# Kernel tuning notes

Measured on AMD Instinct MI355X. Metric: run time of the kernel, lower is better.

Reference implementation:

```python
import jax, jax.numpy as jnp
import numpy as np
import math

EMBED = 1024
HEADS = 16
HEAD_DIM = EMBED // HEADS
B, S = 4, 2048
FF = 4 * EMBED
EPS = 1e-5


def _layernorm(x, g, b):
    mu = jnp.mean(x, axis=-1, keepdims=True)
    var = jnp.mean(jnp.square(x - mu), axis=-1, keepdims=True)
    return (x - mu) * jax.lax.rsqrt(var + EPS) * g + b


def setup_inputs() -> dict:
    key = jax.random.key(0)
    ks = jax.random.split(key, 12)
    sd_e = 1.0 / math.sqrt(EMBED)
    sd_ff = 1.0 / math.sqrt(FF)
    return {
        "x": jax.random.normal(ks[0], (B, S, EMBED), jnp.float32),
        # attention weights stored [in, out] (transposed torch Linear)
        "Wq": jax.random.normal(ks[1], (EMBED, EMBED), jnp.float32) * sd_e,
        "bq": jnp.zeros((EMBED,), jnp.float32),
        "Wk": jax.random.normal(ks[2], (EMBED, EMBED), jnp.float32) * sd_e,
        "bk": jnp.zeros((EMBED,), jnp.float32),
        "Wv": jax.random.normal(ks[3], (EMBED, EMBED), jnp.float32) * sd_e,
        "bv": jnp.zeros((EMBED,), jnp.float32),
        "Wo": jax.random.normal(ks[4], (EMBED, EMBED), jnp.float32) * sd_e,
        "bo": jnp.zeros((EMBED,), jnp.float32),
        "g1": jnp.ones((EMBED,), jnp.float32),
        "beta1": jnp.zeros((EMBED,), jnp.float32),
        "g2": jnp.ones((EMBED,), jnp.float32),
        "beta2": jnp.zeros((EMBED,), jnp.float32),
        "W1": jax.random.normal(ks[5], (EMBED, FF), jnp.float32) * sd_e,
        "b1": jnp.zeros((FF,), jnp.float32),
        "W2": jax.random.normal(ks[6], (FF, EMBED), jnp.float32) * sd_ff,
        "b2": jnp.zeros((EMBED,), jnp.float32),
    }


def reference(x, Wq, bq, Wk, bk, Wv, bv, Wo, bo, g1, beta1, g2, beta2, W1, b1, W2, b2):
    b, s, _ = x.shape
    # --- pre-LN causal self-attention (dropout in eval = identity) ---
    h = _layernorm(x, g1, beta1)
    q = (h @ Wq + bq).reshape(b, s, HEADS, HEAD_DIM)
    k = (h @ Wk + bk).reshape(b, s, HEADS, HEAD_DIM)
    v = (h @ Wv + bv).reshape(b, s, HEADS, HEAD_DIM)
    scores = jnp.einsum("bqhd,bkhd->bhqk", q, k) / math.sqrt(HEAD_DIM)
    causal = jnp.tril(jnp.ones((s, s), bool))
    scores = jnp.where(causal, scores, jnp.float32(-1e8))
    attn = jax.nn.softmax(scores, axis=-1)
    y = jnp.einsum("bhqk,bkhd->bqhd", attn, v).reshape(b, s, EMBED)
    x = x + (y @ Wo + bo)
    # --- GELU MLP (exact erf gelu, torch default) ---
    h2 = _layernorm(x, g2, beta2)
    ff = jax.nn.gelu(h2 @ W1 + b1, approximate=False) @ W2 + b2
    return x + ff
```

## Files before the change

### kernel.cpp

```cpp
#include <hip/hip_runtime.h>
#include <hip/hip_bf16.h>
#include <stdint.h>
#include <math.h>

#define SEQ 2048
#define NTOK 8192
#define EMB 1024
#define NH 16
#define HD 64
#define FFD 4096

using us = unsigned short;
using b8 = __attribute__((ext_vector_type(8))) __bf16;
using f4 = __attribute__((ext_vector_type(4))) float;

__device__ __forceinline__ us f2b(float f) {
  union { float f; uint32_t u; } v; v.f = f;
  uint32_t u = v.u;
  return (us)((u + 0x7fffu + ((u >> 16) & 1u)) >> 16);
}

__device__ __forceinline__ uint32_t pkbf(float a, float b) {
  union { float f; uint32_t u; } x, y; x.f = a; y.f = b;
  return ((x.u + 0x8000u) >> 16) | ((y.u + 0x8000u) & 0xFFFF0000u);
}

__device__ __forceinline__ void async16(void* lds, const void* g) {
  __builtin_amdgcn_global_load_lds(
      (__attribute__((address_space(1))) void*)(uintptr_t)g,
      (__attribute__((address_space(3))) void*)(uintptr_t)lds, 16, 0, 0);
}

#define FENCED_BARRIER() do { asm volatile("" ::: "memory"); \
  __builtin_amdgcn_s_barrier(); asm volatile("" ::: "memory"); } while (0)

__device__ __forceinline__ float gelu_f(float x) {
  const float z = -2.30211416f * x * (1.f + 0.044715f * x * x);
  return x / (1.f + __builtin_amdgcn_exp2f(z));
}

__global__ __launch_bounds__(256)
void transpose_cast(const float* __restrict__ in, us* __restrict__ out, int R, int C) {
  __shared__ float tile[32][33];
  const int bc = blockIdx.x * 32, br = blockIdx.y * 32;
  const int tx = threadIdx.x & 31, ty = threadIdx.x >> 5;
#pragma unroll
  for (int i = 0; i < 32; i += 8)
    tile[ty + i][tx] = in[(size_t)(br + ty + i) * C + bc + tx];
  __syncthreads();
#pragma unroll
  for (int i = 0; i < 32; i += 8)
    out[(size_t)(bc + ty + i) * R + br + tx] = f2b(tile[tx][ty + i]);
}

__global__ void pack_bias(const float* __restrict__ bq, const float* __restrict__ bk,
                          const float* __restrict__ bv, float* __restrict__ o) {
  int i = blockIdx.x * 256 + threadIdx.x;
  o[i] = (i < 1024) ? bq[i] : (i < 2048 ? bk[i - 1024] : bv[i - 2048]);
}

__global__ __launch_bounds__(256)
void ln_kernel(const float* __restrict__ x, const float* __restrict__ g,
               const float* __restrict__ be, us* __restrict__ out) {
  __shared__ float red[8];
  const int row = blockIdx.x, t = threadIdx.x;
  const float4 v = ((const float4*)(x + (size_t)row * EMB))[t];
  float s = v.x + v.y + v.z + v.w;
  float s2 = v.x * v.x + v.y * v.y + v.z * v.z + v.w * v.w;
#pragma unroll
  for (int o = 32; o; o >>= 1) { s += __shfl_down(s, o, 64); s2 += __shfl_down(s2, o, 64); }
  if ((t & 63) == 0) { red[(t >> 6) * 2] = s; red[(t >> 6) * 2 + 1] = s2; }
  __syncthreads();
  const float ts = red[0] + red[2] + red[4] + red[6];
  const float ts2 = red[1] + red[3] + red[5] + red[7];
  const float mu = ts * (1.f / 1024.f);
  const float rs = rsqrtf(ts2 * (1.f / 1024.f) - mu * mu + 1e-5f);
  const float4 gv = ((const float4*)g)[t];
  const float4 bv = ((const float4*)be)[t];
  ushort4 o4;
  o4.x = f2b((v.x - mu) * rs * gv.x + bv.x);
  o4.y = f2b((v.y - mu) * rs * gv.y + bv.y);
  o4.z = f2b((v.z - mu) * rs * gv.z + bv.z);
  o4.w = f2b((v.w - mu) * rs * gv.w + bv.w);
  ((ushort4*)(out + (size_t)row * EMB))[t] = o4;
}

template<int BN>
__global__ __launch_bounds__(512, 2)
void gemm8(const us* __restrict__ A, const us* __restrict__ Bt,
           const float* __restrict__ bias, const float* __restrict__ resid,
           float* __restrict__ outF, us* __restrict__ outB,
           int M, int N, int K, int gelu, int gy) {
  constexpr int NF = BN / 64;
  constexpr int BROWS = BN / 8;
  constexpr int BINSTS = BN / 64;
  __shared__ us As[2][256 * 64];
  __shared__ us Bs[2][BN * 64];

  int bid = blockIdx.x;
  const int cpx = (int)gridDim.x >> 3;
  bid = (bid & 7) * cpx + (bid >> 3);
  const int bx = bid / gy, by = bid - bx * gy;
  const int row0 = bx * 256, col0 = by * BN;

  const int tid = threadIdx.x, w = tid >> 6, lane = tid & 63;
  const int wm = w >> 2, wn = w & 3;
  const int quad = lane >> 4, l15 = lane & 15;

  const int srow = lane >> 3;
  const int soct = (lane & 7) ^ srow;
  const us* Ag = A + (size_t)(row0 + w * 32 + srow) * K + soct * 8;
  const us* Bg = Bt + (size_t)(col0 + w * BROWS + srow) * K + soct * 8;
  const int NT = K >> 6;

  const f4 zf = {0.f, 0.f, 0.f, 0.f};
  f4 acc[8][NF];
#pragma unroll
  for (int i = 0; i < 8; i++)
#pragma unroll
    for (int j = 0; j < NF; j++) acc[i][j] = zf;

  auto STAGE = [&](int buf, int t) {
    const size_t ko = (size_t)t * 64;
#pragma unroll
    for (int i = 0; i < 4; i++)
      async16(&As[buf][(w * 32 + i * 8) * 64], Ag + ko + (size_t)(i * 8) * K);
#pragma unroll
    for (int i = 0; i < BINSTS; i++)
      async16(&Bs[buf][(w * BROWS + i * 8) * 64], Bg + ko + (size_t)(i * 8) * K);
  };

  STAGE(0, 0);
  STAGE(1, 1);
  if constexpr (BN == 256) asm volatile("s_waitcnt vmcnt(8)" ::: "memory");
  else                     asm volatile("s_waitcnt vmcnt(6)" ::: "memory");
  FENCED_BARRIER();

  const int xr = l15 & 7;
  for (int u = 0; u < NT; u++) {
    const int cb = u & 1;
    const us* __restrict__ as = As[cb];
    const us* __restrict__ bs = Bs[cb];
    b8 bf[2][NF];
#pragma unroll
    for (int s = 0; s < 2; s++)
#pragma unroll
      for (int nf = 0; nf < NF; nf++)
        bf[s][nf] = *(const b8*)&bs[(wn * (NF * 16) + nf * 16 + l15) * 64 +
                                    ((((s << 2) + quad) ^ xr) << 3)];
#pragma unroll
    for (int qm = 0; qm < 2; qm++) {
      b8 af[2][4];
#pragma unroll
      for (int s = 0; s < 2; s++)
#pragma unroll
        for (int mi = 0; mi < 4; mi++)
          af[s][mi] = *(const b8*)&as[(wm * 128 + qm * 64 + mi * 16 + l15) * 64 +
                                      ((((s << 2) + quad) ^ xr) << 3)];
      __builtin_amdgcn_s_setprio(1);
#pragma unroll
      for (int s = 0; s < 2; s++)
#pragma unroll
        for (int mi = 0; mi < 4; mi++)
#pragma unroll
          for (int nf = 0; nf < NF; nf++)
            acc[qm * 4 + mi][nf] = __builtin_amdgcn_mfma_f32_16x16x32_bf16(
                af[s][mi], bf[s][nf], acc[qm * 4 + mi][nf], 0, 0, 0);
      __builtin_amdgcn_s_setprio(0);
    }
    asm volatile("s_waitcnt lgkmcnt(0)" ::: "memory");
    FENCED_BARRIER();
    if (u + 2 < NT) {
      STAGE(cb, u + 2);
      if constexpr (BN == 256) asm volatile("s_waitcnt vmcnt(8)" ::: "memory");
      else                     asm volatile("s_waitcnt vmcnt(6)" ::: "memory");
    } else {
      asm volatile("s_waitcnt vmcnt(0)" ::: "memory");
    }
    if (u + 1 < NT) FENCED_BARRIER();
  }

#pragma unroll
  for (int mi8 = 0; mi8 < 8; mi8++) {
#pragma unroll
    for (int nf = 0; nf < NF; nf++) {
      const int gcol = col0 + wn * (NF * 16) + nf * 16 + l15;
      const float bc = bias[gcol];
#pragma unroll
      for (int r = 0; r < 4; r++) {
        const int grow = row0 + wm * 128 + mi8 * 16 + quad * 4 + r;
        float v = acc[mi8][nf][r] + bc;
        if (resid) v += resid[(size_t)grow * N + gcol];
        if (gelu) v = gelu_f(v);
        if (outF) outF[(size_t)grow * N + gcol] = v;
        if (outB) outB[(size_t)grow * N + gcol] = f2b(v);
      }
    }
  }
}

__global__ __launch_bounds__(256, 3)
void attn(const us* __restrict__ qkv, us* __restrict__ y) {
  static const signed char QTM[16] = {15,14,13,12, 10,11,8,9, 5,4,7,6, 0,1,2,3};
  const int bx = blockIdx.x;
  const int bh = bx & 63;
  const int qt = QTM[(bx >> 6) & 15];
  const int bb = bh >> 4, h = bh & 15;
  const int tid = threadIdx.x;
  const int wave = tid >> 6, lane = tid & 63;
  const int quad = lane >> 4, l15 = lane & 15;

  __shared__ us Ks[128 * 64];
  __shared__ us Vt[64 * 132];

  const size_t base = (size_t)bb * SEQ * 3072;
  const int q0 = qt * 128;

  b8 bqf[2][2];
#pragma unroll
  for (int qg = 0; qg < 2; qg++) {
    const us* qp = qkv + base + (size_t)(q0 + wave * 32 + qg * 16 + l15) * 3072 + h * 64 + quad * 8;
    bqf[qg][0] = *(const b8*)qp;
    bqf[qg][1] = *(const b8*)(qp + 32);
  }

  const f4 zf = {0.f, 0.f, 0.f, 0.f};
  f4 o[2][4];
  float mrow[2], lrow[2];
#pragma unroll
  for (int qg = 0; qg < 2; qg++) {
    mrow[qg] = -3.0e38f; lrow[qg] = 0.f;
#pragma unroll
    for (int dg = 0; dg < 4; dg++) o[qg][dg] = zf;
  }

  const int klr = lane >> 3, klc = lane & 7;
  const us* kgbase = qkv + base + (size_t)(wave * 32 + klr) * 3072 + 1024 + h * 64 + ((klc ^ klr) << 3);
  const us* vgbase = qkv + base + (size_t)(2 * lane) * 3072 + 2048 + h * 64 + wave * 8;

  const float sm_scale = 0.125f * 1.44269504088896340736f;

  for (int kt = 0; kt <= qt; kt++) {
    const size_t koff = (size_t)kt * 128 * 3072;
#pragma unroll
    for (int op = 0; op < 4; op++)
      async16(&Ks[(wave * 32 + op * 8) * 64], kgbase + koff + (size_t)op * 8 * 3072);
    {
      union { float4 f; us u[8]; } v0, v1, v2, v3;
      v0.f = *(const float4*)(vgbase + koff);
      v1.f = *(const float4*)(vgbase + koff + 3072);
      v2.f = *(const float4*)(vgbase + koff + 32);
      v3.f = *(const float4*)(vgbase + koff + 3072 + 32);
#pragma unroll
      for (int j = 0; j < 8; j++) {
        *(uint32_t*)&Vt[(wave * 8 + j) * 132 + 2 * lane] =
            (uint32_t)v0.u[j] | ((uint32_t)v1.u[j] << 16);
        *(uint32_t*)&Vt[(32 + wave * 8 + j) * 132 + 2 * lane] =
            (uint32_t)v2.u[j] | ((uint32_t)v3.u[j] << 16);
      }
    }
    __syncthreads();

    f4 sacc[2][8];
#pragma unroll
    for (int c = 0; c < 8; c++) {
      const int krow = (c * 16 + l15) * 64;
      const int sw = l15 & 7;
      const b8 ak0 = *(const b8*)&Ks[krow + ((quad ^ sw) << 3)];
      const b8 ak1 = *(const b8*)&Ks[krow + (((quad ^ 4) ^ sw) << 3)];
#pragma unroll
      for (int qg = 0; qg < 2; qg++) {
        f4 s = __builtin_amdgcn_mfma_f32_16x16x32_bf16(ak0, bqf[qg][0], zf, 0, 0, 0);
        sacc[qg][c] = __builtin_amdgcn_mfma_f32_16x16x32_bf16(ak1, bqf[qg][1], s, 0, 0, 0);
      }
    }

    uint32_t pf[2][16];
    float alpha[2];
#pragma unroll
    for (int qg = 0; qg < 2; qg++) {
      const int q_in = wave * 32 + qg * 16 + l15;
#pragma unroll
      for (int c = 0; c < 8; c++)
#pragma unroll
        for (int r = 0; r < 4; r++) {
          float v = sacc[qg][c][r] * sm_scale;
          if (kt == qt && (c * 16 + quad * 4 + r) > q_in) v = -3.0e38f;
          sacc[qg][c][r] = v;
        }
      float mx = sacc[qg][0][0];
#pragma unroll
      for (int c = 0; c < 8; c++)
#pragma unroll
        for (int r = 0; r < 4; r++) mx = fmaxf(mx, sacc[qg][c][r]);
      mx = fmaxf(mx, __shfl_xor(mx, 16, 64));
      mx = fmaxf(mx, __shfl_xor(mx, 32, 64));
      const float mnew = fmaxf(mrow[qg], mx);
      alpha[qg] = __builtin_amdgcn_exp2f(mrow[qg] - mnew);
      mrow[qg] = mnew;
      float rs = 0.f;
#pragma unroll
      for (int c = 0; c < 8; c++) {
        const float p0 = __builtin_amdgcn_exp2f(sacc[qg][c][0] - mnew);
        const float p1 = __builtin_amdgcn_exp2f(sacc[qg][c][1] - mnew);
        const float p2 = __builtin_amdgcn_exp2f(sacc[qg][c][2] - mnew);
        const float p3 = __builtin_amdgcn_exp2f(sacc[qg][c][3] - mnew);
        rs += (p0 + p1) + (p2 + p3);
        pf[qg][c * 2] = pkbf(p0, p1);
        pf[qg][c * 2 + 1] = pkbf(p2, p3);
      }
      rs += __shfl_xor(rs, 16, 64);
      rs += __shfl_xor(rs, 32, 64);
      lrow[qg] = lrow[qg] * alpha[qg] + rs;
#pragma unroll
      for (int r = 0; r < 4; r++) {
        const float ar = __shfl(alpha[qg], quad * 4 + r, 64);
#pragma unroll
        for (int dg = 0; dg < 4; dg++) o[qg][dg][r] *= ar;
      }
    }

#pragma unroll
    for (int c = 0; c < 8; c++) {
      union { uint32_t w[4]; b8 v; } af0, af1;
      af0.w[0] = pf[0][c * 2]; af0.w[1] = pf[0][c * 2 + 1]; af0.w[2] = 0u; af0.w[3] = 0u;
      af1.w[0] = pf[1][c * 2]; af1.w[1] = pf[1][c * 2 + 1]; af1.w[2] = 0u; af1.w[3] = 0u;
#pragma unroll
      for (int dg = 0; dg < 4; dg++) {
        const uint2 vd = *(const uint2*)&Vt[(dg * 16 + l15) * 132 + c * 16 + quad * 4];
        union { uint32_t w[4]; b8 v; } vb;
        vb.w[0] = vd.x; vb.w[1] = vd.y; vb.w[2] = 0u; vb.w[3] = 0u;
        o[0][dg] = __builtin_amdgcn_mfma_f32_16x16x32_bf16(af0.v, vb.v, o[0][dg], 0, 0, 0);
        o[1][dg] = __builtin_amdgcn_mfma_f32_16x16x32_bf16(af1.v, vb.v, o[1][dg], 0, 0, 0);
      }
    }
    __syncthreads();
  }

#pragma unroll
  for (int qg = 0; qg < 2; qg++) {
    float lr[4];
#pragma unroll
    for (int r = 0; r < 4; r++) lr[r] = __shfl(lrow[qg], quad * 4 + r, 64);
#pragma unroll
    for (int dg = 0; dg < 4; dg++)
#pragma unroll
      for (int r = 0; r < 4; r++) {
        const int gq = q0 + wave * 32 + qg * 16 + quad * 4 + r;
        y[(size_t)(bb * SEQ + gq) * EMB + h * 64 + dg * 16 + l15] = f2b(o[qg][dg][r] / lr[r]);
      }
  }
}

extern "C" void kernel_launch(void* const* d_in, const int* in_sizes, int n_in,
                              void* d_out, int out_size, void* d_ws, size_t ws_size,
                              hipStream_t stream) {
  const float* x = (const float*)d_in[0];
  const float* Wq = (const float*)d_in[1];
  const float* bq = (const float*)d_in[2];
  const float* Wk = (const float*)d_in[3];
  const float* bk = (const float*)d_in[4];
  const float* Wv = (const float*)d_in[5];
  const float* bv = (const float*)d_in[6];
  const float* Wo = (const float*)d_in[7];
  const float* bo = (const float*)d_in[8];
  const float* g1 = (const float*)d_in[9];
  const float* be1 = (const float*)d_in[10];
  const float* g2 = (const float*)d_in[11];
  const float* be2 = (const float*)d_in[12];
  const float* W1 = (const float*)d_in[13];
  const float* b1 = (const float*)d_in[14];
  const float* W2 = (const float*)d_in[15];
  const float* b2 = (const float*)d_in[16];
  float* out = (float*)d_out;

  char* ws = (char*)d_ws;
  const size_t MB = 1024ull * 1024ull;
  us* WqkvT = (us*)(ws + 0);
  us* WoT   = (us*)(ws + 6 * MB);
  us* W1T   = (us*)(ws + 8 * MB);
  us* W2T   = (us*)(ws + 16 * MB);
  us* hbuf  = (us*)(ws + 24 * MB);
  us* qkvb  = (us*)(ws + 40 * MB);
  us* ybuf  = (us*)(ws + 88 * MB);
  float* x1 = (float*)(ws + 104 * MB);
  us* h2    = (us*)(ws + 136 * MB);
  us* ff1   = (us*)(ws + 24 * MB);
  float* bqkv = (float*)(ws + 152 * MB);

  transpose_cast<<<dim3(32, 32), 256, 0, stream>>>(Wq, WqkvT, 1024, 1024);
  transpose_cast<<<dim3(32, 32), 256, 0, stream>>>(Wk, WqkvT + 1024 * 1024, 1024, 1024);
  transpose_cast<<<dim3(32, 32), 256, 0, stream>>>(Wv, WqkvT + 2 * 1024 * 1024, 1024, 1024);
  transpose_cast<<<dim3(32, 32), 256, 0, stream>>>(Wo, WoT, 1024, 1024);
  transpose_cast<<<dim3(128, 32), 256, 0, stream>>>(W1, W1T, 1024, 4096);
  transpose_cast<<<dim3(32, 128), 256, 0, stream>>>(W2, W2T, 4096, 1024);
  pack_bias<<<12, 256, 0, stream>>>(bq, bk, bv, bqkv);

  ln_kernel<<<NTOK, 256, 0, stream>>>(x, g1, be1, hbuf);
  gemm8<128><<<dim3(32 * 24), 512, 0, stream>>>(hbuf, WqkvT, bqkv, nullptr, nullptr, qkvb,
                                                NTOK, 3072, 1024, 0, 24);
  attn<<<1024, 256, 0, stream>>>(qkvb, ybuf);
  gemm8<128><<<dim3(32 * 8), 512, 0, stream>>>(ybuf, WoT, bo, x, x1, nullptr,
                                               NTOK, 1024, 1024, 0, 8);
  ln_kernel<<<NTOK, 256, 0, stream>>>(x1, g2, be2, h2);
  gemm8<256><<<dim3(32 * 16), 512, 0, stream>>>(h2, W1T, b1, nullptr, nullptr, ff1,
                                                NTOK, 4096, 1024, 1, 16);
  gemm8<128><<<dim3(32 * 8), 512, 0, stream>>>(ff1, W2T, b2, x1, out, nullptr,
                                               NTOK, 1024, 4096, 0, 8);
}
```

Measured before the change: 570.8 us.

## Split GEMM into 256x256 and 128x256 kernels with quarter-tile interleaved staging

Replaces the templated gemm8 with two specialized kernels. gemm256 handles the QKV and FFN1 projections with 256x256 tiles (QKV previously used 256x128). gemm128 handles the Wo and FFN2 projections with 128x256 tiles. Each K-step is split into sub-phases that issue async global loads for the next tiles between MFMA groups, with a barrier around each phase, so memory traffic overlaps compute. The epilogues are also specialized. The trade-off is more barriers per K-step, more complex vmcnt accounting, and different grid sizes and wave counts for the smaller-N GEMMs.

```diff
diff --git a/kernel.cpp b/kernel.cpp
--- a/kernel.cpp
+++ b/kernel.cpp
@@ -85,118 +85,294 @@
   ((ushort4*)(out + (size_t)row * EMB))[t] = o4;
 }
 
-template<int BN>
 __global__ __launch_bounds__(512, 2)
-void gemm8(const us* __restrict__ A, const us* __restrict__ Bt,
-           const float* __restrict__ bias, const float* __restrict__ resid,
-           float* __restrict__ outF, us* __restrict__ outB,
-           int M, int N, int K, int gelu, int gy) {
-  constexpr int NF = BN / 64;
-  constexpr int BROWS = BN / 8;
-  constexpr int BINSTS = BN / 64;
+void gemm256(const us* __restrict__ A, const us* __restrict__ Bt,
+             const float* __restrict__ bias, us* __restrict__ outB,
+             int N, int K, int gelu, int gy) {
   __shared__ us As[2][256 * 64];
-  __shared__ us Bs[2][BN * 64];
+  __shared__ us Bs[2][256 * 64];
 
   int bid = blockIdx.x;
   const int cpx = (int)gridDim.x >> 3;
   bid = (bid & 7) * cpx + (bid >> 3);
   const int bx = bid / gy, by = bid - bx * gy;
-  const int row0 = bx * 256, col0 = by * BN;
+  const int row0 = bx * 256, col0 = by * 256;
 
   const int tid = threadIdx.x, w = tid >> 6, lane = tid & 63;
   const int wm = w >> 2, wn = w & 3;
   const int quad = lane >> 4, l15 = lane & 15;
-
-  const int srow = lane >> 3;
-  const int soct = (lane & 7) ^ srow;
-  const us* Ag = A + (size_t)(row0 + w * 32 + srow) * K + soct * 8;
-  const us* Bg = Bt + (size_t)(col0 + w * BROWS + srow) * K + soct * 8;
+  const int xr = l15 & 7;
+
+  const int u0 = w * 2, u1 = u0 + 1;
+  const int ar0 = ((u0 & 7) << 3) + ((u0 >> 3) << 7);
+  const int ar1 = ((u1 & 7) << 3) + ((u1 >> 3) << 7);
+  const int br0 = ((u0 & 3) << 3) + ((u0 >> 2) << 6);
+  const int br1 = ((u1 & 3) << 3) + ((u1 >> 2) << 6);
+  const int lrow = lane >> 3;
+  const int loct = ((lane & 7) ^ lrow) << 3;
+  const us* Ag0 = A + (size_t)(row0 + ar0 + lrow) * K + loct;
+  const us* Ag1 = A + (size_t)(row0 + ar1 + lrow) * K + loct;
+  const us* Bg0 = Bt + (size_t)(col0 + br0 + lrow) * K + loct;
+  const us* Bg1 = Bt + (size_t)(col0 + br1 + lrow) * K + loct;
   const int NT = K >> 6;
 
   const f4 zf = {0.f, 0.f, 0.f, 0.f};
-  f4 acc[8][NF];
+  f4 acc[8][4];
 #pragma unroll
   for (int i = 0; i < 8; i++)
 #pragma unroll
-    for (int j = 0; j < NF; j++) acc[i][j] = zf;
-
-  auto STAGE = [&](int buf, int t) {
-    const size_t ko = (size_t)t * 64;
-#pragma unroll
-    for (int i = 0; i < 4; i++)
-      async16(&As[buf][(w * 32 + i * 8) * 64], Ag + ko + (size_t)(i * 8) * K);
-#pragma unroll
-    for (int i = 0; i < BINSTS; i++)
-      async16(&Bs[buf][(w * BROWS + i * 8) * 64], Bg + ko + (size_t)(i * 8) * K);
+    for (int j = 0; j < 4; j++) acc[i][j] = zf;
+
+  auto stgA = [&](int buf, int t, int mh) {
+    const size_t go = (size_t)(mh << 6) * K + ((size_t)t << 6);
+    async16(&As[buf][(ar0 + (mh << 6)) << 6], Ag0 + go);
+    async16(&As[buf][(ar1 + (mh << 6)) << 6], Ag1 + go);
   };
-
-  STAGE(0, 0);
-  STAGE(1, 1);
-  if constexpr (BN == 256) asm volatile("s_waitcnt vmcnt(8)" ::: "memory");
-  else                     asm volatile("s_waitcnt vmcnt(6)" ::: "memory");
+  auto stgB = [&](int buf, int t, int nh) {
+    const size_t go = (size_t)(nh << 5) * K + ((size_t)t << 6);
+    async16(&Bs[buf][(br0 + (nh << 5)) << 6], Bg0 + go);
+    async16(&Bs[buf][(br1 + (nh << 5)) << 6], Bg1 + go);
+  };
+
+  stgA(0, 0, 0); stgB(0, 0, 0); stgB(0, 0, 1); stgA(0, 0, 1);
+  stgA(1, 1, 0); stgB(1, 1, 0); stgB(1, 1, 1);
+  asm volatile("s_waitcnt vmcnt(6)" ::: "memory");
   FENCED_BARRIER();
 
-  const int xr = l15 & 7;
-  for (int u = 0; u < NT; u++) {
-    const int cb = u & 1;
-    const us* __restrict__ as = As[cb];
-    const us* __restrict__ bs = Bs[cb];
-    b8 bf[2][NF];
+  for (int t = 0; t < NT; t++) {
+    const int cur = t & 1, nxt = cur ^ 1;
+    const us* __restrict__ as = As[cur];
+    const us* __restrict__ bs = Bs[cur];
+    b8 af[2][4], bf0[2][2], bf1[2][2];
+
+#pragma unroll
+    for (int s = 0; s < 2; s++) {
+      const int po = (((s << 2) + quad) ^ xr) << 3;
+#pragma unroll
+      for (int mi = 0; mi < 4; mi++)
+        af[s][mi] = *(const b8*)&as[(wm * 128 + mi * 16 + l15) * 64 + po];
+#pragma unroll
+      for (int nf = 0; nf < 2; nf++)
+        bf0[s][nf] = *(const b8*)&bs[(wn * 64 + nf * 16 + l15) * 64 + po];
+    }
+    if (t + 1 < NT) stgA(nxt, t + 1, 1);
+    FENCED_BARRIER();
+    asm volatile("s_waitcnt lgkmcnt(0)" ::: "memory");
+    __builtin_amdgcn_s_setprio(1);
 #pragma unroll
     for (int s = 0; s < 2; s++)
 #pragma unroll
-      for (int nf = 0; nf < NF; nf++)
-        bf[s][nf] = *(const b8*)&bs[(wn * (NF * 16) + nf * 16 + l15) * 64 +
-                                    ((((s << 2) + quad) ^ xr) << 3)];
-#pragma unroll
-    for (int qm = 0; qm < 2; qm++) {
-      b8 af[2][4];
-#pragma unroll
-      for (int s = 0; s < 2; s++)
-#pragma unroll
-        for (int mi = 0; mi < 4; mi++)
-          af[s][mi] = *(const b8*)&as[(wm * 128 + qm * 64 + mi * 16 + l15) * 64 +
-                                      ((((s << 2) + quad) ^ xr) << 3)];
-      __builtin_amdgcn_s_setprio(1);
-#pragma unroll
-      for (int s = 0; s < 2; s++)
-#pragma unroll
-        for (int mi = 0; mi < 4; mi++)
-#pragma unroll
-          for (int nf = 0; nf < NF; nf++)
-            acc[qm * 4 + mi][nf] = __builtin_amdgcn_mfma_f32_16x16x32_bf16(
-                af[s][mi], bf[s][nf], acc[qm * 4 + mi][nf], 0, 0, 0);
-      __builtin_amdgcn_s_setprio(0);
-    }
+      for (int mi = 0; mi < 4; mi++)
+#pragma unroll
+        for (int nf = 0; nf < 2; nf++)
+          acc[mi][nf] = __builtin_amdgcn_mfma_f32_16x16x32_bf16(af[s][mi], bf0[s][nf], acc[mi][nf], 0, 0, 0);
+    __builtin_amdgcn_s_setprio(0);
+    FENCED_BARRIER();
+
+#pragma unroll
+    for (int s = 0; s < 2; s++) {
+      const int po = (((s << 2) + quad) ^ xr) << 3;
+#pragma unroll
+      for (int nf = 0; nf < 2; nf++)
+        bf1[s][nf] = *(const b8*)&bs[(wn * 64 + 32 + nf * 16 + l15) * 64 + po];
+    }
+    if (t + 2 < NT) stgA(cur, t + 2, 0);
+    FENCED_BARRIER();
     asm volatile("s_waitcnt lgkmcnt(0)" ::: "memory");
-    FENCED_BARRIER();
-    if (u + 2 < NT) {
-      STAGE(cb, u + 2);
-      if constexpr (BN == 256) asm volatile("s_waitcnt vmcnt(8)" ::: "memory");
-      else                     asm volatile("s_waitcnt vmcnt(6)" ::: "memory");
+    __builtin_amdgcn_s_setprio(1);
+#pragma unroll
+    for (int s = 0; s < 2; s++)
+#pragma unroll
+      for (int mi = 0; mi < 4; mi++)
+#pragma unroll
+        for (int nf = 0; nf < 2; nf++)
+          acc[mi][2 + nf] = __builtin_amdgcn_mfma_f32_16x16x32_bf16(af[s][mi], bf1[s][nf], acc[mi][2 + nf], 0, 0, 0);
+    __builtin_amdgcn_s_setprio(0);
+    FENCED_BARRIER();
+
+#pragma unroll
+    for (int s = 0; s < 2; s++) {
+      const int po = (((s << 2) + quad) ^ xr) << 3;
+#pragma unroll
+      for (int mi = 0; mi < 4; mi++)
+        af[s][mi] = *(const b8*)&as[(wm * 128 + 64 + mi * 16 + l15) * 64 + po];
+    }
+    if (t + 2 < NT) stgB(cur, t + 2, 0);
+    FENCED_BARRIER();
+    asm volatile("s_waitcnt lgkmcnt(0)" ::: "memory");
+    __builtin_amdgcn_s_setprio(1);
+#pragma unroll
+    for (int s = 0; s < 2; s++)
+#pragma unroll
+      for (int mi = 0; mi < 4; mi++)
+#pragma unroll
+        for (int nf = 0; nf < 2; nf++)
+          acc[4 + mi][nf] = __builtin_amdgcn_mfma_f32_16x16x32_bf16(af[s][mi], bf0[s][nf], acc[4 + mi][nf], 0, 0, 0);
+    __builtin_amdgcn_s_setprio(0);
+    FENCED_BARRIER();
+
+    if (t + 2 < NT) {
+      stgB(cur, t + 2, 1);
+      asm volatile("s_waitcnt vmcnt(6)" ::: "memory");
     } else {
       asm volatile("s_waitcnt vmcnt(0)" ::: "memory");
     }
-    if (u + 1 < NT) FENCED_BARRIER();
+    FENCED_BARRIER();
+    __builtin_amdgcn_s_setprio(1);
+#pragma unroll
+    for (int s = 0; s < 2; s++)
+#pragma unroll
+      for (int mi = 0; mi < 4; mi++)
+#pragma unroll
+        for (int nf = 0; nf < 2; nf++)
+          acc[4 + mi][2 + nf] = __builtin_amdgcn_mfma_f32_16x16x32_bf16(af[s][mi], bf1[s][nf], acc[4 + mi][2 + nf], 0, 0, 0);
+    __builtin_amdgcn_s_setprio(0);
+    FENCED_BARRIER();
   }
 
 #pragma unroll
-  for (int mi8 = 0; mi8 < 8; mi8++) {
-#pragma unroll
-    for (int nf = 0; nf < NF; nf++) {
-      const int gcol = col0 + wn * (NF * 16) + nf * 16 + l15;
+  for (int mi8 = 0; mi8 < 8; mi8++)
+#pragma unroll
+    for (int nf = 0; nf < 4; nf++) {
+      const int gcol = col0 + wn * 64 + nf * 16 + l15;
       const float bc = bias[gcol];
 #pragma unroll
       for (int r = 0; r < 4; r++) {
         const int grow = row0 + wm * 128 + mi8 * 16 + quad * 4 + r;
         float v = acc[mi8][nf][r] + bc;
-        if (resid) v += resid[(size_t)grow * N + gcol];
         if (gelu) v = gelu_f(v);
-        if (outF) outF[(size_t)grow * N + gcol] = v;
-        if (outB) outB[(size_t)grow * N + gcol] = f2b(v);
-      }
-    }
+        outB[(size_t)grow * N + gcol] = f2b(v);
+      }
+    }
+}
+
+__global__ __launch_bounds__(512, 2)
+void gemm128(const us* __restrict__ A, const us* __restrict__ Bt,
+             const float* __restrict__ bias, const float* __restrict__ resid,
+             float* __restrict__ outF, int N, int K, int gy) {
+  __shared__ us As[2][128 * 64];
+  __shared__ us Bs[2][256 * 64];
+
+  int bid = blockIdx.x;
+  const int cpx = (int)gridDim.x >> 3;
+  bid = (bid & 7) * cpx + (bid >> 3);
+  const int bx = bid / gy, by = bid - bx * gy;
+  const int row0 = bx * 128, col0 = by * 256;
+
+  const int tid = threadIdx.x, w = tid >> 6, lane = tid & 63;
+  const int wm = w >> 2, wn = w & 3;
+  const int quad = lane >> 4, l15 = lane & 15;
+  const int xr = l15 & 7;
+
+  const int u0 = w * 2, u1 = u0 + 1;
+  const int aR0 = u0 << 3, aR1 = u1 << 3;
+  const int bR0 = ((u0 & 3) << 3) + ((u0 >> 2) << 6);
+  const int bR1 = ((u1 & 3) << 3) + ((u1 >> 2) << 6);
+  const int lrow = lane >> 3;
+  const int loct = ((lane & 7) ^ lrow) << 3;
+  const us* Ag0 = A + (size_t)(row0 + aR0 + lrow) * K + loct;
+  const us* Ag1 = A + (size_t)(row0 + aR1 + lrow) * K + loct;
+  const us* Bg0 = Bt + (size_t)(col0 + bR0 + lrow) * K + loct;
+  const us* Bg1 = Bt + (size_t)(col0 + bR1 + lrow) * K + loct;
+  const int NT = K >> 6;
+
+  const f4 zf = {0.f, 0.f, 0.f, 0.f};
+  f4 acc[4][4];
+#pragma unroll
+  for (int i = 0; i < 4; i++)
+#pragma unroll
+    for (int j = 0; j < 4; j++) acc[i][j] = zf;
+
+  auto stgA = [&](int buf, int t) {
+    const size_t go = (size_t)t << 6;
+    async16(&As[buf][aR0 << 6], Ag0 + go);
+    async16(&As[buf][aR1 << 6], Ag1 + go);
+  };
+  auto stgB = [&](int buf, int t, int nh) {
+    const size_t go = (size_t)(nh << 5) * K + ((size_t)t << 6);
+    async16(&Bs[buf][(bR0 + (nh << 5)) << 6], Bg0 + go);
+    async16(&Bs[buf][(bR1 + (nh << 5)) << 6], Bg1 + go);
+  };
+
+  stgA(0, 0); stgB(0, 0, 0); stgB(0, 0, 1);
+  stgA(1, 1); stgB(1, 1, 0);
+  asm volatile("s_waitcnt vmcnt(6)" ::: "memory");
+  FENCED_BARRIER();
+
+  for (int t = 0; t < NT; t++) {
+    const int cur = t & 1, nxt = cur ^ 1;
+    const us* __restrict__ as = As[cur];
+    const us* __restrict__ bs = Bs[cur];
+    b8 af[2][4], bf0[2][2], bf1[2][2];
+
+#pragma unroll
+    for (int s = 0; s < 2; s++) {
+      const int po = (((s << 2) + quad) ^ xr) << 3;
+#pragma unroll
+      for (int mi = 0; mi < 4; mi++)
+        af[s][mi] = *(const b8*)&as[(wm * 64 + mi * 16 + l15) * 64 + po];
+#pragma unroll
+      for (int nf = 0; nf < 2; nf++)
+        bf0[s][nf] = *(const b8*)&bs[(wn * 64 + nf * 16 + l15) * 64 + po];
+    }
+    if (t + 1 < NT) {
+      stgB(nxt, t + 1, 1);
+      asm volatile("s_waitcnt vmcnt(6)" ::: "memory");
+    } else {
+      asm volatile("s_waitcnt vmcnt(0)" ::: "memory");
+    }
+    FENCED_BARRIER();
+    asm volatile("s_waitcnt lgkmcnt(0)" ::: "memory");
+    __builtin_amdgcn_s_setprio(1);
+#pragma unroll
+    for (int s = 0; s < 2; s++)
+#pragma unroll
+      for (int mi = 0; mi < 4; mi++)
+#pragma unroll
+        for (int nf = 0; nf < 2; nf++)
+          acc[mi][nf] = __builtin_amdgcn_mfma_f32_16x16x32_bf16(af[s][mi], bf0[s][nf], acc[mi][nf], 0, 0, 0);
+    __builtin_amdgcn_s_setprio(0);
+    FENCED_BARRIER();
+
+#pragma unroll
+    for (int s = 0; s < 2; s++) {
+      const int po = (((s << 2) + quad) ^ xr) << 3;
+#pragma unroll
+      for (int nf = 0; nf < 2; nf++)
+        bf1[s][nf] = *(const b8*)&bs[(wn * 64 + 32 + nf * 16 + l15) * 64 + po];
+    }
+    if (t + 2 < NT) {
+      stgA(cur, t + 2); stgB(cur, t + 2, 0);
+      asm volatile("s_waitcnt vmcnt(6)" ::: "memory");
+    } else {
+      asm volatile("s_waitcnt vmcnt(2)" ::: "memory");
+    }
+    FENCED_BARRIER();
+    asm volatile("s_waitcnt lgkmcnt(0)" ::: "memory");
+    __builtin_amdgcn_s_setprio(1);
+#pragma unroll
+    for (int s = 0; s < 2; s++)
+#pragma unroll
+      for (int mi = 0; mi < 4; mi++)
+#pragma unroll
+        for (int nf = 0; nf < 2; nf++)
+          acc[mi][2 + nf] = __builtin_amdgcn_mfma_f32_16x16x32_bf16(af[s][mi], bf1[s][nf], acc[mi][2 + nf], 0, 0, 0);
+    __builtin_amdgcn_s_setprio(0);
+    FENCED_BARRIER();
   }
+
+#pragma unroll
+  for (int mi = 0; mi < 4; mi++)
+#pragma unroll
+    for (int nf = 0; nf < 4; nf++) {
+      const int gcol = col0 + wn * 64 + nf * 16 + l15;
+      const float bc = bias[gcol];
+#pragma unroll
+      for (int r = 0; r < 4; r++) {
+        const int grow = row0 + wm * 64 + mi * 16 + quad * 4 + r;
+        outF[(size_t)grow * N + gcol] = acc[mi][nf][r] + bc + resid[(size_t)grow * N + gcol];
+      }
+    }
 }
 
 __global__ __launch_bounds__(256, 3)
@@ -397,14 +573,10 @@
   pack_bias<<<12, 256, 0, stream>>>(bq, bk, bv, bqkv);
 
   ln_kernel<<<NTOK, 256, 0, stream>>>(x, g1, be1, hbuf);
-  gemm8<128><<<dim3(32 * 24), 512, 0, stream>>>(hbuf, WqkvT, bqkv, nullptr, nullptr, qkvb,
-                                                NTOK, 3072, 1024, 0, 24);
+  gemm256<<<dim3(384), 512, 0, stream>>>(hbuf, WqkvT, bqkv, qkvb, 3072, 1024, 0, 12);
   attn<<<1024, 256, 0, stream>>>(qkvb, ybuf);
-  gemm8<128><<<dim3(32 * 8), 512, 0, stream>>>(ybuf, WoT, bo, x, x1, nullptr,
-                                               NTOK, 1024, 1024, 0, 8);
+  gemm128<<<dim3(256), 512, 0, stream>>>(ybuf, WoT, bo, x, x1, 1024, 1024, 4);
   ln_kernel<<<NTOK, 256, 0, stream>>>(x1, g2, be2, h2);
-  gemm8<256><<<dim3(32 * 16), 512, 0, stream>>>(h2, W1T, b1, nullptr, nullptr, ff1,
-                                                NTOK, 4096, 1024, 1, 16);
-  gemm8<128><<<dim3(32 * 8), 512, 0, stream>>>(ff1, W2T, b2, x1, out, nullptr,
-                                               NTOK, 1024, 4096, 0, 8);
-}
+  gemm256<<<dim3(512), 512, 0, stream>>>(h2, W1T, b1, ff1, 4096, 1024, 1, 16);
+  gemm128<<<dim3(256), 512, 0, stream>>>(ff1, W2T, b2, x1, out, 1024, 4096, 4);
+}
```

After: 540.8 us. -5.3%, faster.
